# Optimization experiments

Hardware: AMD Instinct MI355X
Metric: run time of the kernel (lower is better)

## Reference

```python
import jax, jax.numpy as jnp
import numpy as np

N, E, H, HEADS, EDIM, DEG_VOCAB, DEG_DIM = 50000, 320000, 128, 4, 8, 100, 16


def _layer_norm(x, g, b, eps=1e-5):
    m = jnp.mean(x, axis=-1, keepdims=True)
    v = jnp.mean(jnp.square(x - m), axis=-1, keepdims=True)
    return (x - m) / jnp.sqrt(v + eps) * g + b


def setup_inputs() -> dict:
    key = jax.random.key(0)
    ks = jax.random.split(key, 24)
    s = 0.05
    inp = {
        "x": jax.random.normal(ks[0], (N, H), jnp.float32),
        "edge_index": jax.random.randint(ks[1], (2, E), 0, N, jnp.int64),
        "edge_attr": jax.random.normal(ks[2], (E, EDIM), jnp.float32),
        "node_degrees": jax.random.randint(ks[3], (N,), 0, DEG_VOCAB, jnp.int64),
        "check_node_mask": jax.random.randint(ks[4], (N,), 0, 2, jnp.int32).astype(bool),
        # GATv2Conv params (bias=False): lin_l, lin_r, lin_edge, att
        "Wl": jax.random.normal(ks[5], (H, HEADS * H), jnp.float32) * s,
        "Wr": jax.random.normal(ks[6], (H, HEADS * H), jnp.float32) * s,
        "We": jax.random.normal(ks[7], (EDIM, HEADS * H), jnp.float32) * s,
        "att": jax.random.normal(ks[8], (HEADS, H), jnp.float32) * s,
        # check_transform: Linear->Tanh->Linear->LayerNorm
        "ct_W1": jax.random.normal(ks[9], (H, H), jnp.float32) * s,
        "ct_b1": jnp.zeros((H,), jnp.float32),
        "ct_W2": jax.random.normal(ks[10], (H, H), jnp.float32) * s,
        "ct_b2": jnp.zeros((H,), jnp.float32),
        "ct_g": jnp.ones((H,), jnp.float32),
        "ct_beta": jnp.zeros((H,), jnp.float32),
        # degree embedding + gate MLP
        "deg_emb": jax.random.normal(ks[11], (DEG_VOCAB, DEG_DIM), jnp.float32) * s,
        "dg_W1": jax.random.normal(ks[12], (H + DEG_DIM, H), jnp.float32) * s,
        "dg_b1": jnp.zeros((H,), jnp.float32),
        "dg_g": jnp.ones((H,), jnp.float32),
        "dg_beta": jnp.zeros((H,), jnp.float32),
        "dg_W2": jax.random.normal(ks[13], (H, H), jnp.float32) * s,
        "dg_b2": jnp.zeros((H,), jnp.float32),
        # final layer norm
        "ln_g": jnp.ones((H,), jnp.float32),
        "ln_beta": jnp.zeros((H,), jnp.float32),
    }
    return inp


def reference(x, edge_index, edge_attr, node_degrees, check_node_mask,
              Wl, Wr, We, att,
              ct_W1, ct_b1, ct_W2, ct_b2, ct_g, ct_beta,
              deg_emb, dg_W1, dg_b1, dg_g, dg_beta, dg_W2, dg_b2,
              ln_g, ln_beta):
    n = x.shape[0]
    # --- check-node transform (applied where mask) ---
    ct = jnp.tanh(x @ ct_W1 + ct_b1) @ ct_W2 + ct_b2
    ct = _layer_norm(ct, ct_g, ct_beta)
    x_t = jnp.where(check_node_mask[:, None], ct, x)

    # --- GATv2Conv with add_self_loops=True, fill_value='mean' for edge_attr ---
    src, dst = edge_index[0], edge_index[1]
    cnt = jax.ops.segment_sum(jnp.ones((edge_attr.shape[0],), edge_attr.dtype), dst, n)
    loop_attr = jax.ops.segment_sum(edge_attr, dst, n) / jnp.maximum(cnt, 1.0)[:, None]
    ar = jnp.arange(n, dtype=src.dtype)
    src_f = jnp.concatenate([src, ar])
    dst_f = jnp.concatenate([dst, ar])
    ea_f = jnp.concatenate([edge_attr, loop_attr], axis=0)

    xl = (x_t @ Wl).reshape(n, HEADS, H)   # source-side (x_j)
    xr = (x_t @ Wr).reshape(n, HEADS, H)   # target-side (x_i)
    ee = (ea_f @ We).reshape(-1, HEADS, H)

    s = jax.nn.leaky_relu(xl[src_f] + xr[dst_f] + ee, 0.2)  # [Ef, heads, H]
    alpha = jnp.einsum('ehd,hd->eh', s, att)
    amax = jax.lax.stop_gradient(jax.ops.segment_max(alpha, dst_f, n))
    ealpha = jnp.exp(alpha - amax[dst_f])
    denom = jax.ops.segment_sum(ealpha, dst_f, n)
    alpha = ealpha / denom[dst_f]           # segment softmax over dst
    # dropout skipped (eval mode)
    out = jax.ops.segment_sum(alpha[:, :, None] * xl[src_f], dst_f, n)  # [N, heads, H]
    x_c2v = out.mean(axis=1)                # concat=False -> mean over heads; bias=False

    # --- degree gating ---
    deg = jnp.clip(node_degrees, 0, DEG_VOCAB - 1)
    df = deg_emb[deg]
    g = jnp.concatenate([x_c2v, df], axis=-1) @ dg_W1 + dg_b1
    g = jax.nn.relu(_layer_norm(g, dg_g, dg_beta)) @ dg_W2 + dg_b2
    x_c2v = x_c2v * jax.nn.sigmoid(g)

    return _layer_norm(x_c2v, ln_g, ln_beta)
```

## Files before the change

### kernel.cpp

```cpp
#include <hip/hip_runtime.h>


#define HDIM 128
#define NHEADS 4
#define EDIM_ 8
#define WHID (NHEADS * HDIM)

typedef __attribute__((ext_vector_type(8))) short short8;
typedef __attribute__((ext_vector_type(4))) float f32x4;

__device__ __forceinline__ float bf2f(unsigned short u) {
    return __uint_as_float(((unsigned int)u) << 16);
}
__device__ __forceinline__ unsigned short f2bf(float f) {
    unsigned int x = __float_as_uint(f);
    unsigned int r = x + 0x7FFFu + ((x >> 16) & 1u);
    return (unsigned short)(r >> 16);
}
__device__ __forceinline__ short8 pack8(float4 a, float4 b) {
    short8 v;
    v[0] = (short)f2bf(a.x); v[1] = (short)f2bf(a.y);
    v[2] = (short)f2bf(a.z); v[3] = (short)f2bf(a.w);
    v[4] = (short)f2bf(b.x); v[5] = (short)f2bf(b.y);
    v[6] = (short)f2bf(b.z); v[7] = (short)f2bf(b.w);
    return v;
}

__global__ __launch_bounds__(256) void k_prep(
    const float* __restrict__ Wl, const float* __restrict__ Wr,
    const float* __restrict__ ctW1, const float* __restrict__ ctW2,
    const float* __restrict__ dgW1, const float* __restrict__ dgW2,
    const float* __restrict__ demb,
    unsigned short* __restrict__ Wbt,
    unsigned short* __restrict__ ctW1t, unsigned short* __restrict__ ctW2t,
    unsigned short* __restrict__ dgW1t, unsigned short* __restrict__ dgW2t,
    float* __restrict__ demb2)
{
    int idx = blockIdx.x * 256 + threadIdx.x;
    if (idx < 131072) {
        int nn = idx >> 7, k = idx & 127;
        const float* W = (nn < WHID) ? Wl : Wr;
        Wbt[idx] = f2bf(W[(size_t)k * WHID + (nn & (WHID - 1))]);
    } else if (idx < 131072 + 65536) {
        int i = idx - 131072;
        int sel = i >> 14;
        int j = i & 16383;
        int n = j >> 7, k = j & 127;
        const float* src = (sel == 0) ? ctW1 : (sel == 1) ? ctW2
                         : (sel == 2) ? dgW1 : dgW2;
        unsigned short* dst = (sel == 0) ? ctW1t : (sel == 1) ? ctW2t
                            : (sel == 2) ? dgW1t : dgW2t;
        dst[j] = f2bf(src[k * 128 + n]);
    } else if (idx < 131072 + 65536 + 12800) {
        int i = idx - 131072 - 65536;
        int d = i >> 7, n = i & 127;
        float s = 0.f;
#pragma unroll
        for (int j = 0; j < 16; j++)
            s += demb[d * 16 + j] * dgW1[(128 + j) * 128 + n];
        demb2[i] = s;
    }
}

__global__ __launch_bounds__(256) void k_ct2(
    const float* __restrict__ x, const int* __restrict__ mask,
    const unsigned short* __restrict__ W1t, const float* __restrict__ b1,
    const unsigned short* __restrict__ W2t, const float* __restrict__ b2,
    const float* __restrict__ g, const float* __restrict__ be,
    unsigned short* __restrict__ xt, int Nn)
{
    __shared__ __align__(16) char Xs[16384];
    __shared__ __align__(16) char Bs[32768];
    __shared__ __align__(16) char Hs[16384];
    __shared__ float rsum[2][64], rsq[2][64];

    const int tid = threadIdx.x;
    const int l = tid & 63, w = tid >> 6;
    const int wm = w >> 1, wn = w & 1;
    const int l15 = l & 15, lq = l >> 4;
    const int row0 = blockIdx.x * 64;

    {
        int r = tid >> 2, q = tid & 3;
        int grow = min(row0 + r, Nn - 1);
        const float* xp = x + (size_t)grow * 128 + q * 32;
        int sb = r * 256, sw = (r & 7) << 4;
#pragma unroll
        for (int u = 0; u < 4; u++) {
            float4 f0 = *reinterpret_cast<const float4*>(xp + u * 8);
            float4 f1 = *reinterpret_cast<const float4*>(xp + u * 8 + 4);
            *reinterpret_cast<short8*>(Xs + sb + (((q * 4 + u) * 16) ^ sw)) = pack8(f0, f1);
        }
    }
    {
        int cr = tid >> 1, h2 = tid & 1;
        int sb = cr * 256, sw = (cr & 7) << 4;
        const unsigned short* wp = W1t + cr * 128 + h2 * 64;
#pragma unroll
        for (int u = 0; u < 8; u++) {
            short8 v = *reinterpret_cast<const short8*>(wp + u * 8);
            *reinterpret_cast<short8*>(Bs + sb + (((h2 * 8 + u) * 16) ^ sw)) = v;
        }
    }
    __syncthreads();

    f32x4 acc[2][4];
#pragma unroll
    for (int i = 0; i < 2; i++)
#pragma unroll
        for (int j = 0; j < 4; j++) acc[i][j] = (f32x4){0.f, 0.f, 0.f, 0.f};
#pragma unroll
    for (int kc = 0; kc < 4; kc++) {
        int ck = (kc * 4 + lq) * 16;
        short8 a[2], b[4];
#pragma unroll
        for (int i = 0; i < 2; i++) {
            int m = wm * 32 + i * 16 + l15;
            a[i] = *reinterpret_cast<const short8*>(Xs + m * 256 + (ck ^ ((m & 7) << 4)));
        }
#pragma unroll
        for (int j = 0; j < 4; j++) {
            int c = wn * 64 + j * 16 + l15;
            b[j] = *reinterpret_cast<const short8*>(Bs + c * 256 + (ck ^ ((c & 7) << 4)));
        }
#pragma unroll
        for (int i = 0; i < 2; i++)
#pragma unroll
            for (int j = 0; j < 4; j++)
                acc[i][j] = __builtin_amdgcn_mfma_f32_16x16x32_bf16(a[i], b[j], acc[i][j], 0, 0, 0);
    }

    {
        float b1v[4];
#pragma unroll
        for (int j = 0; j < 4; j++) b1v[j] = b1[wn * 64 + j * 16 + l15];
#pragma unroll
        for (int i = 0; i < 2; i++)
#pragma unroll
            for (int j = 0; j < 4; j++) {
                int col = wn * 64 + j * 16 + l15;
                int cb = (col >> 3) * 16, ce = (col & 7) * 2;
#pragma unroll
                for (int r = 0; r < 4; r++) {
                    int m = wm * 32 + i * 16 + lq * 4 + r;
                    float v = tanhf(acc[i][j][r] + b1v[j]);
                    *reinterpret_cast<unsigned short*>(
                        Hs + m * 256 + (cb ^ ((m & 7) << 4)) + ce) = f2bf(v);
                }
            }
    }
    __syncthreads();

    {
        int cr = tid >> 1, h2 = tid & 1;
        int sb = cr * 256, sw = (cr & 7) << 4;
        const unsigned short* wp = W2t + cr * 128 + h2 * 64;
#pragma unroll
        for (int u = 0; u < 8; u++) {
            short8 v = *reinterpret_cast<const short8*>(wp + u * 8);
            *reinterpret_cast<short8*>(Bs + sb + (((h2 * 8 + u) * 16) ^ sw)) = v;
        }
    }
    __syncthreads();

    f32x4 acc2[2][4];
#pragma unroll
    for (int i = 0; i < 2; i++)
#pragma unroll
        for (int j = 0; j < 4; j++) acc2[i][j] = (f32x4){0.f, 0.f, 0.f, 0.f};
#pragma unroll
    for (int kc = 0; kc < 4; kc++) {
        int ck = (kc * 4 + lq) * 16;
        short8 a[2], b[4];
#pragma unroll
        for (int i = 0; i < 2; i++) {
            int m = wm * 32 + i * 16 + l15;
            a[i] = *reinterpret_cast<const short8*>(Hs + m * 256 + (ck ^ ((m & 7) << 4)));
        }
#pragma unroll
        for (int j = 0; j < 4; j++) {
            int c = wn * 64 + j * 16 + l15;
            b[j] = *reinterpret_cast<const short8*>(Bs + c * 256 + (ck ^ ((c & 7) << 4)));
        }
#pragma unroll
        for (int i = 0; i < 2; i++)
#pragma unroll
            for (int j = 0; j < 4; j++)
                acc2[i][j] = __builtin_amdgcn_mfma_f32_16x16x32_bf16(a[i], b[j], acc2[i][j], 0, 0, 0);
    }

    float v2[2][4][4];
    {
        float b2v[4];
#pragma unroll
        for (int j = 0; j < 4; j++) b2v[j] = b2[wn * 64 + j * 16 + l15];
#pragma unroll
        for (int i = 0; i < 2; i++)
#pragma unroll
            for (int j = 0; j < 4; j++)
#pragma unroll
                for (int r = 0; r < 4; r++) v2[i][j][r] = acc2[i][j][r] + b2v[j];
    }
#pragma unroll
    for (int i = 0; i < 2; i++)
#pragma unroll
        for (int r = 0; r < 4; r++) {
            float p = 0.f, q = 0.f;
#pragma unroll
            for (int j = 0; j < 4; j++) { float t = v2[i][j][r]; p += t; q += t * t; }
#pragma unroll
            for (int off = 1; off <= 8; off <<= 1) {
                p += __shfl_xor(p, off);
                q += __shfl_xor(q, off);
            }
            if (l15 == 0) {
                int m = wm * 32 + i * 16 + lq * 4 + r;
                rsum[wn][m] = p; rsq[wn][m] = q;
            }
        }
    __syncthreads();

    {
        float gv[4], bev[4];
#pragma unroll
        for (int j = 0; j < 4; j++) {
            int col = wn * 64 + j * 16 + l15;
            gv[j] = g[col]; bev[j] = be[col];
        }
#pragma unroll
        for (int i = 0; i < 2; i++)
#pragma unroll
            for (int r = 0; r < 4; r++) {
                int m = wm * 32 + i * 16 + lq * 4 + r;
                int grow = row0 + m;
                float s = rsum[0][m] + rsum[1][m];
                float q2 = rsq[0][m] + rsq[1][m];
                float mn = s * (1.f / 128.f);
                float va = q2 * (1.f / 128.f) - mn * mn;
                float rs = rsqrtf(va + 1e-5f);
                int mk = (grow < Nn) ? mask[grow] : 0;
#pragma unroll
                for (int j = 0; j < 4; j++) {
                    int col = wn * 64 + j * 16 + l15;
                    float ln = (v2[i][j][r] - mn) * rs * gv[j] + bev[j];
                    unsigned short xo = *reinterpret_cast<const unsigned short*>(
                        Xs + m * 256 + (((col >> 3) * 16) ^ ((m & 7) << 4)) + (col & 7) * 2);
                    unsigned short res = mk ? f2bf(ln) : xo;
                    if (grow < Nn) xt[(size_t)grow * 128 + col] = res;
                }
            }
    }
}

__global__ __launch_bounds__(256) void k_gemm_xlr(
    const unsigned short* __restrict__ xt,
    const unsigned short* __restrict__ Wbt,
    unsigned short* __restrict__ xlr, int Nn)
{
    __shared__ __align__(16) char smem[65536];
    char* Asb = smem;
    char* Bsb = smem + 32768;

    const int tid = threadIdx.x;
    const int bm = blockIdx.x, bn = blockIdx.y;
    const int l = tid & 63;
    const int w = tid >> 6;
    const int wm = w >> 1, wn = w & 1;

    {
        const int c = tid & 15;
        const int rb = tid >> 4;
#pragma unroll
        for (int i = 0; i < 8; i++) {
            int r = i * 16 + rb;
            int swz = (c * 16) ^ ((r & 7) << 4);
            int grow = bm * 128 + r;
            grow = (grow < Nn) ? grow : (Nn - 1);
            short8 va = *reinterpret_cast<const short8*>(xt + (size_t)grow * 128 + c * 8);
            *reinterpret_cast<short8*>(Asb + r * 256 + swz) = va;
            int nrow = bn * 128 + r;
            short8 vb = *reinterpret_cast<const short8*>(Wbt + (size_t)nrow * 128 + c * 8);
            *reinterpret_cast<short8*>(Bsb + r * 256 + swz) = vb;
        }
    }
    __syncthreads();

    f32x4 acc[4][4];
#pragma unroll
    for (int i = 0; i < 4; i++)
#pragma unroll
        for (int j = 0; j < 4; j++) acc[i][j] = (f32x4){0.f, 0.f, 0.f, 0.f};

    const int l15 = l & 15, lq = l >> 4;
#pragma unroll
    for (int kc = 0; kc < 4; kc++) {
        short8 a[4], b[4];
        int ck = (kc * 4 + lq) * 16;
#pragma unroll
        for (int i = 0; i < 4; i++) {
            int m = wm * 64 + i * 16 + l15;
            a[i] = *reinterpret_cast<const short8*>(Asb + m * 256 + (ck ^ ((m & 7) << 4)));
        }
#pragma unroll
        for (int j = 0; j < 4; j++) {
            int nn = wn * 64 + j * 16 + l15;
            b[j] = *reinterpret_cast<const short8*>(Bsb + nn * 256 + (ck ^ ((nn & 7) << 4)));
        }
#pragma unroll
        for (int i = 0; i < 4; i++)
#pragma unroll
            for (int j = 0; j < 4; j++)
                acc[i][j] = __builtin_amdgcn_mfma_f32_16x16x32_bf16(a[i], b[j], acc[i][j], 0, 0, 0);
    }

#pragma unroll
    for (int i = 0; i < 4; i++) {
        int mg0 = bm * 128 + wm * 64 + i * 16 + lq * 4;
#pragma unroll
        for (int j = 0; j < 4; j++) {
            int ng = bn * 128 + wn * 64 + j * 16 + l15;
#pragma unroll
            for (int r = 0; r < 4; r++) {
                int mg = mg0 + r;
                if (mg < Nn)
                    xlr[(size_t)mg * 1024 + ng] = f2bf(acc[i][j][r]);
            }
        }
    }
}

__global__ __launch_bounds__(256) void k_hist(
    const int* __restrict__ ei, const float* __restrict__ eattr,
    float* __restrict__ loop_sum, int* __restrict__ cnt, int Ee)
{
    int gid = blockIdx.x * 256 + threadIdx.x;
    int e = gid >> 3, j = gid & 7;
    if (e >= Ee) return;
    int dst = ei[Ee + e];
    if (j == 0) atomicAdd(&cnt[dst], 1);
    atomicAdd(&loop_sum[(size_t)dst * EDIM_ + j], eattr[(size_t)e * EDIM_ + j]);
}

__global__ __launch_bounds__(256) void k_loopdiv(
    float* __restrict__ loop_sum, const int* __restrict__ cnt, int Nn)
{
    int gid = blockIdx.x * 256 + threadIdx.x;
    if (gid >= Nn * EDIM_) return;
    float c = fmaxf((float)cnt[gid >> 3], 1.f);
    loop_sum[gid] /= c;
}

__global__ __launch_bounds__(256) void k_scanA(const int* __restrict__ cnt,
                                               int* __restrict__ bsum, int Nn)
{
    __shared__ int s[256];
    int i = blockIdx.x * 256 + threadIdx.x;
    int v = (i < Nn) ? cnt[i] + 1 : 0;
    s[threadIdx.x] = v;
    __syncthreads();
    for (int off = 128; off; off >>= 1) {
        if (threadIdx.x < off) s[threadIdx.x] += s[threadIdx.x + off];
        __syncthreads();
    }
    if (threadIdx.x == 0) bsum[blockIdx.x] = s[0];
}

__global__ __launch_bounds__(256) void k_scanB(const int* __restrict__ bsum,
                                               int* __restrict__ boff, int NB)
{
    __shared__ int s[256];
    int tid = threadIdx.x;
    int v = (tid < NB) ? bsum[tid] : 0;
    s[tid] = v;
    __syncthreads();
    for (int off = 1; off < 256; off <<= 1) {
        int t = (tid >= off) ? s[tid - off] : 0;
        __syncthreads();
        s[tid] += t;
        __syncthreads();
    }
    if (tid < NB) boff[tid] = s[tid] - v;
}

__global__ __launch_bounds__(256) void k_scanC(const int* __restrict__ cnt,
                                               const int* __restrict__ boff,
                                               int* __restrict__ offs, int Nn)
{
    __shared__ int s[256];
    int tid = threadIdx.x;
    int i = blockIdx.x * 256 + tid;
    int v = (i < Nn) ? cnt[i] + 1 : 0;
    s[tid] = v;
    __syncthreads();
    for (int off = 1; off < 256; off <<= 1) {
        int t = (tid >= off) ? s[tid - off] : 0;
        __syncthreads();
        s[tid] += t;
        __syncthreads();
    }
    if (i < Nn) {
        int incl = s[tid];
        offs[i] = boff[blockIdx.x] + incl - v;
        if (i == Nn - 1) offs[Nn] = boff[blockIdx.x] + incl;
    }
}

__global__ __launch_bounds__(256) void k_scatter(
    const int* __restrict__ ei, const int* __restrict__ offs,
    int* __restrict__ cursor, int* __restrict__ csr_src,
    int* __restrict__ csr_eid, int Ee, int Nn)
{
    int gid = blockIdx.x * 256 + threadIdx.x;
    if (gid < Ee) {
        int dst = ei[Ee + gid];
        int pos = offs[dst] + atomicAdd(&cursor[dst], 1);
        csr_src[pos] = ei[gid];
        csr_eid[pos] = gid;
    } else if (gid < Ee + Nn) {
        int n = gid - Ee;
        int pos = offs[n + 1] - 1;
        csr_src[pos] = n;
        csr_eid[pos] = Ee + n;
    }
}

__global__ __launch_bounds__(256) void k_attn5(
    const float* __restrict__ eattr, const float* __restrict__ loop_attr,
    const unsigned short* __restrict__ xlr,
    const float* __restrict__ We, const float* __restrict__ att,
    const int* __restrict__ offs, const int* __restrict__ csr_src,
    const int* __restrict__ csr_eid,
    float* __restrict__ xc2v, int Nn, int Ee)
{
    const int tid  = threadIdx.x;
    const int wv   = tid >> 6;
    const int lane = tid & 63;
    const int hp   = wv & 1;
    const int par  = wv >> 1;
    const int n    = blockIdx.x;
    const int hloc = lane >> 5;
    const int col  = (hp * 2 + hloc) * HDIM + (lane & 31) * 4;

    __shared__ float sacc[4][256];
    __shared__ float slsum[4][2];

    float a[4], xr[4], we[EDIM_][4];
#pragma unroll
    for (int k = 0; k < 4; k++) a[k] = att[col + k];
    {
        ushort4 uxr = *reinterpret_cast<const ushort4*>(
            &xlr[(size_t)n * 1024 + WHID + col]);
        xr[0] = bf2f(uxr.x); xr[1] = bf2f(uxr.y);
        xr[2] = bf2f(uxr.z); xr[3] = bf2f(uxr.w);
    }
#pragma unroll
    for (int j = 0; j < EDIM_; j++)
#pragma unroll
        for (int k = 0; k < 4; k++) we[j][k] = We[j * WHID + col + k];

    const int s0 = offs[n], s1 = offs[n + 1];
    float lsum = 0.f, acc[4] = {0.f, 0.f, 0.f, 0.f};

    auto score = [&](int src, int eid, float xl[4]) -> float {
        const float* ep = (eid < Ee) ? eattr + (size_t)eid * EDIM_
                                     : loop_attr + (size_t)n * EDIM_;
        float4 ea = *reinterpret_cast<const float4*>(ep);
        float4 eb = *reinterpret_cast<const float4*>(ep + 4);
        ushort4 u = *reinterpret_cast<const ushort4*>(
            &xlr[(size_t)src * 1024 + col]);
        xl[0] = bf2f(u.x); xl[1] = bf2f(u.y);
        xl[2] = bf2f(u.z); xl[3] = bf2f(u.w);
        float p = 0.f;
#pragma unroll
        for (int k = 0; k < 4; k++) {
            float s = xl[k] + xr[k];
            s = fmaf(ea.x, we[0][k], s); s = fmaf(ea.y, we[1][k], s);
            s = fmaf(ea.z, we[2][k], s); s = fmaf(ea.w, we[3][k], s);
            s = fmaf(eb.x, we[4][k], s); s = fmaf(eb.y, we[5][k], s);
            s = fmaf(eb.z, we[6][k], s); s = fmaf(eb.w, we[7][k], s);
            s = (s > 0.f) ? s : 0.2f * s;
            p = fmaf(s, a[k], p);
        }
        return p;
    };

    int i = s0 + par;
    for (; i + 2 < s1; i += 4) {
        int src0 = csr_src[i],     eid0 = csr_eid[i];
        int src1 = csr_src[i + 2], eid1 = csr_eid[i + 2];
        float xl0[4], xl1[4];
        float p0 = score(src0, eid0, xl0);
        float p1 = score(src1, eid1, xl1);
#pragma unroll
        for (int off = 16; off; off >>= 1) {
            p0 += __shfl_xor(p0, off);
            p1 += __shfl_xor(p1, off);
        }
        float w0 = __expf(p0), w1 = __expf(p1);
        lsum += w0 + w1;
#pragma unroll
        for (int k = 0; k < 4; k++)
            acc[k] = fmaf(w0, xl0[k], fmaf(w1, xl1[k], acc[k]));
    }
    if (i < s1) {
        int src0 = csr_src[i], eid0 = csr_eid[i];
        float xl0[4];
        float p0 = score(src0, eid0, xl0);
#pragma unroll
        for (int off = 16; off; off >>= 1) p0 += __shfl_xor(p0, off);
        float w0 = __expf(p0);
        lsum += w0;
#pragma unroll
        for (int k = 0; k < 4; k++) acc[k] = fmaf(w0, xl0[k], acc[k]);
    }

#pragma unroll
    for (int k = 0; k < 4; k++)
        sacc[wv][hloc * 128 + (lane & 31) * 4 + k] = acc[k];
    if ((lane & 31) == 0) slsum[wv][hloc] = lsum;
    __syncthreads();

    if (tid < HDIM) {
        float o = 0.f;
#pragma unroll
        for (int p2 = 0; p2 < 2; p2++) {
#pragma unroll
            for (int hl = 0; hl < 2; hl++) {
                float num = sacc[p2][hl * 128 + tid] + sacc[p2 + 2][hl * 128 + tid];
                float den = slsum[p2][hl] + slsum[p2 + 2][hl];
                o += num / den;
            }
        }
        xc2v[(size_t)n * HDIM + tid] = 0.25f * o;
    }
}

__global__ __launch_bounds__(256) void k_gate2(
    const float* __restrict__ xc2v, const int* __restrict__ degs,
    const float* __restrict__ demb2,
    const unsigned short* __restrict__ W1t, const float* __restrict__ b1,
    const float* __restrict__ g1v, const float* __restrict__ be1,
    const unsigned short* __restrict__ W2t, const float* __restrict__ b2,
    const float* __restrict__ lng, const float* __restrict__ lnbe,
    float* __restrict__ out, int Nn)
{
    __shared__ __align__(16) char Vs[16384];
    __shared__ __align__(16) char Bs[32768];
    __shared__ __align__(16) char Hs[16384];
    __shared__ float rsum[2][64], rsq[2][64];

    const int tid = threadIdx.x;
    const int l = tid & 63, w = tid >> 6;
    const int wm = w >> 1, wn = w & 1;
    const int l15 = l & 15, lq = l >> 4;
    const int row0 = blockIdx.x * 64;

    {
        int r = tid >> 2, q = tid & 3;
        int grow = min(row0 + r, Nn - 1);
        const float* xp = xc2v + (size_t)grow * 128 + q * 32;
        int sb = r * 256, sw = (r & 7) << 4;
#pragma unroll
        for (int u = 0; u < 4; u++) {
            float4 f0 = *reinterpret_cast<const float4*>(xp + u * 8);
            float4 f1 = *reinterpret_cast<const float4*>(xp + u * 8 + 4);
            *reinterpret_cast<short8*>(Vs + sb + (((q * 4 + u) * 16) ^ sw)) = pack8(f0, f1);
        }
    }
    {
        int cr = tid >> 1, h2 = tid & 1;
        int sb = cr * 256, sw = (cr & 7) << 4;
        const unsigned short* wp = W1t + cr * 128 + h2 * 64;
#pragma unroll
        for (int u = 0; u < 8; u++) {
            short8 v = *reinterpret_cast<const short8*>(wp + u * 8);
            *reinterpret_cast<short8*>(Bs + sb + (((h2 * 8 + u) * 16) ^ sw)) = v;
        }
    }
    __syncthreads();

    f32x4 acc[2][4];
#pragma unroll
    for (int i = 0; i < 2; i++)
#pragma unroll
        for (int j = 0; j < 4; j++) acc[i][j] = (f32x4){0.f, 0.f, 0.f, 0.f};
#pragma unroll
    for (int kc = 0; kc < 4; kc++) {
        int ck = (kc * 4 + lq) * 16;
        short8 a[2], b[4];
#pragma unroll
        for (int i = 0; i < 2; i++) {
            int m = wm * 32 + i * 16 + l15;
            a[i] = *reinterpret_cast<const short8*>(Vs + m * 256 + (ck ^ ((m & 7) << 4)));
        }
#pragma unroll
        for (int j = 0; j < 4; j++) {
            int c = wn * 64 + j * 16 + l15;
            b[j] = *reinterpret_cast<const short8*>(Bs + c * 256 + (ck ^ ((c & 7) << 4)));
        }
#pragma unroll
        for (int i = 0; i < 2; i++)
#pragma unroll
            for (int j = 0; j < 4; j++)
                acc[i][j] = __builtin_amdgcn_mfma_f32_16x16x32_bf16(a[i], b[j], acc[i][j], 0, 0, 0);
    }

    float z[2][4][4];
    {
        float b1v[4];
        int colv[4];
#pragma unroll
        for (int j = 0; j < 4; j++) {
            colv[j] = wn * 64 + j * 16 + l15;
            b1v[j] = b1[colv[j]];
        }
#pragma unroll
        for (int i = 0; i < 2; i++)
#pragma unroll
            for (int r = 0; r < 4; r++) {
                int m = wm * 32 + i * 16 + lq * 4 + r;
                int grow = row0 + m;
                int dg = (grow < Nn) ? degs[grow] : 0;
                dg = min(max(dg, 0), 99);
#pragma unroll
                for (int j = 0; j < 4; j++)
                    z[i][j][r] = acc[i][j][r] + b1v[j] + demb2[dg * 128 + colv[j]];
            }
    }
#pragma unroll
    for (int i = 0; i < 2; i++)
#pragma unroll
        for (int r = 0; r < 4; r++) {
            float p = 0.f, q = 0.f;
#pragma unroll
            for (int j = 0; j < 4; j++) { float t = z[i][j][r]; p += t; q += t * t; }
#pragma unroll
            for (int off = 1; off <= 8; off <<= 1) {
                p += __shfl_xor(p, off);
                q += __shfl_xor(q, off);
            }
            if (l15 == 0) {
                int m = wm * 32 + i * 16 + lq * 4 + r;
                rsum[wn][m] = p; rsq[wn][m] = q;
            }
        }
    __syncthreads();

    {
        float gv[4], bev[4];
#pragma unroll
        for (int j = 0; j < 4; j++) {
            int col = wn * 64 + j * 16 + l15;
            gv[j] = g1v[col]; bev[j] = be1[col];
        }
#pragma unroll
        for (int i = 0; i < 2; i++)
#pragma unroll
            for (int r = 0; r < 4; r++) {
                int m = wm * 32 + i * 16 + lq * 4 + r;
                float s = rsum[0][m] + rsum[1][m];
                float q2 = rsq[0][m] + rsq[1][m];
                float mn = s * (1.f / 128.f);
                float va = q2 * (1.f / 128.f) - mn * mn;
                float rs = rsqrtf(va + 1e-5f);
#pragma unroll
                for (int j = 0; j < 4; j++) {
                    int col = wn * 64 + j * 16 + l15;
                    float h = fmaxf((z[i][j][r] - mn) * rs * gv[j] + bev[j], 0.f);
                    *reinterpret_cast<unsigned short*>(
                        Hs + m * 256 + (((col >> 3) * 16) ^ ((m & 7) << 4)) + (col & 7) * 2) = f2bf(h);
                }
            }
    }
    __syncthreads();

    {
        int cr = tid >> 1, h2 = tid & 1;
        int sb = cr * 256, sw = (cr & 7) << 4;
        const unsigned short* wp = W2t + cr * 128 + h2 * 64;
#pragma unroll
        for (int u = 0; u < 8; u++) {
            short8 v = *reinterpret_cast<const short8*>(wp + u * 8);
            *reinterpret_cast<short8*>(Bs + sb + (((h2 * 8 + u) * 16) ^ sw)) = v;
        }
    }
    __syncthreads();

    f32x4 acc2[2][4];
#pragma unroll
    for (int i = 0; i < 2; i++)
#pragma unroll
        for (int j = 0; j < 4; j++) acc2[i][j] = (f32x4){0.f, 0.f, 0.f, 0.f};
#pragma unroll
    for (int kc = 0; kc < 4; kc++) {
        int ck = (kc * 4 + lq) * 16;
        short8 a[2], b[4];
#pragma unroll
        for (int i = 0; i < 2; i++) {
            int m = wm * 32 + i * 16 + l15;
            a[i] = *reinterpret_cast<const short8*>(Hs + m * 256 + (ck ^ ((m & 7) << 4)));
        }
#pragma unroll
        for (int j = 0; j < 4; j++) {
            int c = wn * 64 + j * 16 + l15;
            b[j] = *reinterpret_cast<const short8*>(Bs + c * 256 + (ck ^ ((c & 7) << 4)));
        }
#pragma unroll
        for (int i = 0; i < 2; i++)
#pragma unroll
            for (int j = 0; j < 4; j++)
                acc2[i][j] = __builtin_amdgcn_mfma_f32_16x16x32_bf16(a[i], b[j], acc2[i][j], 0, 0, 0);
    }

    float y[2][4][4];
    {
        float b2v[4];
#pragma unroll
        for (int j = 0; j < 4; j++) b2v[j] = b2[wn * 64 + j * 16 + l15];
#pragma unroll
        for (int i = 0; i < 2; i++)
#pragma unroll
            for (int j = 0; j < 4; j++) {
                int col = wn * 64 + j * 16 + l15;
                int cb = (col >> 3) * 16, ce = (col & 7) * 2;
#pragma unroll
                for (int r = 0; r < 4; r++) {
                    int m = wm * 32 + i * 16 + lq * 4 + r;
                    float zz = acc2[i][j][r] + b2v[j];
                    float sg = 1.f / (1.f + __expf(-zz));
                    float vv = bf2f(*reinterpret_cast<const unsigned short*>(
                        Vs + m * 256 + (cb ^ ((m & 7) << 4)) + ce));
                    y[i][j][r] = vv * sg;
                }
            }
    }
#pragma unroll
    for (int i = 0; i < 2; i++)
#pragma unroll
        for (int r = 0; r < 4; r++) {
            float p = 0.f, q = 0.f;
#pragma unroll
            for (int j = 0; j < 4; j++) { float t = y[i][j][r]; p += t; q += t * t; }
#pragma unroll
            for (int off = 1; off <= 8; off <<= 1) {
                p += __shfl_xor(p, off);
                q += __shfl_xor(q, off);
            }
            if (l15 == 0) {
                int m = wm * 32 + i * 16 + lq * 4 + r;
                rsum[wn][m] = p; rsq[wn][m] = q;
            }
        }
    __syncthreads();

    {
        float gv[4], bev[4];
#pragma unroll
        for (int j = 0; j < 4; j++) {
            int col = wn * 64 + j * 16 + l15;
            gv[j] = lng[col]; bev[j] = lnbe[col];
        }
#pragma unroll
        for (int i = 0; i < 2; i++)
#pragma unroll
            for (int r = 0; r < 4; r++) {
                int m = wm * 32 + i * 16 + lq * 4 + r;
                int grow = row0 + m;
                float s = rsum[0][m] + rsum[1][m];
                float q2 = rsq[0][m] + rsq[1][m];
                float mn = s * (1.f / 128.f);
                float va = q2 * (1.f / 128.f) - mn * mn;
                float rs = rsqrtf(va + 1e-5f);
#pragma unroll
                for (int j = 0; j < 4; j++) {
                    int col = wn * 64 + j * 16 + l15;
                    float o = (y[i][j][r] - mn) * rs * gv[j] + bev[j];
                    if (grow < Nn) out[(size_t)grow * 128 + col] = o;
                }
            }
    }
}

extern "C" void kernel_launch(void* const* d_in, const int* in_sizes, int n_in,
                              void* d_out, int out_size, void* d_ws, size_t ws_size,
                              hipStream_t stream)
{
    const float* x      = (const float*)d_in[0];
    const int*   ei     = (const int*)d_in[1];
    const float* eattr  = (const float*)d_in[2];
    const int*   degs   = (const int*)d_in[3];
    const int*   maskp  = (const int*)d_in[4];
    const float* Wl     = (const float*)d_in[5];
    const float* Wr     = (const float*)d_in[6];
    const float* We     = (const float*)d_in[7];
    const float* att    = (const float*)d_in[8];
    const float* ct_W1  = (const float*)d_in[9];
    const float* ct_b1  = (const float*)d_in[10];
    const float* ct_W2  = (const float*)d_in[11];
    const float* ct_b2  = (const float*)d_in[12];
    const float* ct_g   = (const float*)d_in[13];
    const float* ct_be  = (const float*)d_in[14];
    const float* demb   = (const float*)d_in[15];
    const float* dg_W1  = (const float*)d_in[16];
    const float* dg_b1  = (const float*)d_in[17];
    const float* dg_g   = (const float*)d_in[18];
    const float* dg_be  = (const float*)d_in[19];
    const float* dg_W2  = (const float*)d_in[20];
    const float* dg_b2  = (const float*)d_in[21];
    const float* ln_g   = (const float*)d_in[22];
    const float* ln_be  = (const float*)d_in[23];
    float* out = (float*)d_out;

    const int N = in_sizes[0] / HDIM;
    const int E = in_sizes[1] / 2;

    char* w = (char*)d_ws;
    size_t off = 0;
    auto alloc = [&](size_t bytes) -> char* {
        char* p = w + off;
        off = (off + bytes + 255) & ~(size_t)255;
        return p;
    };
    unsigned short* xt    = (unsigned short*)alloc((size_t)N * HDIM * 2);
    unsigned short* xlr   = (unsigned short*)alloc((size_t)N * 1024 * 2);
    unsigned short* Wbt   = (unsigned short*)alloc((size_t)1024 * HDIM * 2);
    unsigned short* ctW1t = (unsigned short*)alloc(16384 * 2);
    unsigned short* ctW2t = (unsigned short*)alloc(16384 * 2);
    unsigned short* dgW1t = (unsigned short*)alloc(16384 * 2);
    unsigned short* dgW2t = (unsigned short*)alloc(16384 * 2);
    float* demb2          = (float*)alloc(12800 * 4);
    float* loop_attr      = (float*)alloc((size_t)N * EDIM_ * 4);
    int*   cnt            = (int*)alloc((size_t)N * 4);
    int*   cursor         = (int*)alloc((size_t)N * 4);
    int*   offs           = (int*)alloc((size_t)(N + 1) * 4);
    int*   bsum           = (int*)alloc(256 * 4);
    int*   boff           = (int*)alloc(256 * 4);
    int*   csr_src        = (int*)alloc((size_t)(E + N) * 4);
    int*   csr_eid        = (int*)alloc((size_t)(E + N) * 4);
    float* xc2v           = (float*)alloc((size_t)N * HDIM * 4);
    (void)ws_size;

    hipMemsetAsync(cnt, 0, (size_t)N * 4, stream);
    hipMemsetAsync(cursor, 0, (size_t)N * 4, stream);
    hipMemsetAsync(loop_attr, 0, (size_t)N * EDIM_ * 4, stream);

    const int NB = (N + 255) / 256;

    k_prep<<<(131072 + 65536 + 12800 + 255) / 256, 256, 0, stream>>>(
        Wl, Wr, ct_W1, ct_W2, dg_W1, dg_W2, demb,
        Wbt, ctW1t, ctW2t, dgW1t, dgW2t, demb2);
    k_ct2<<<(N + 63) / 64, 256, 0, stream>>>(x, maskp, ctW1t, ct_b1,
                                             ctW2t, ct_b2, ct_g, ct_be, xt, N);
    {
        dim3 grid((N + 127) / 128, 8);
        k_gemm_xlr<<<grid, 256, 0, stream>>>(xt, Wbt, xlr, N);
    }
    k_hist<<<((size_t)E * EDIM_ + 255) / 256, 256, 0, stream>>>(ei, eattr, loop_attr, cnt, E);
    k_loopdiv<<<((size_t)N * EDIM_ + 255) / 256, 256, 0, stream>>>(loop_attr, cnt, N);
    k_scanA<<<NB, 256, 0, stream>>>(cnt, bsum, N);
    k_scanB<<<1, 256, 0, stream>>>(bsum, boff, NB);
    k_scanC<<<NB, 256, 0, stream>>>(cnt, boff, offs, N);
    k_scatter<<<(E + N + 255) / 256, 256, 0, stream>>>(ei, offs, cursor,
                                                       csr_src, csr_eid, E, N);
    k_attn5<<<N, 256, 0, stream>>>(eattr, loop_attr, xlr, We, att,
                                   offs, csr_src, csr_eid, xc2v, N, E);
    k_gate2<<<(N + 63) / 64, 256, 0, stream>>>(xc2v, degs, demb2,
                                               dgW1t, dg_b1, dg_g, dg_be,
                                               dgW2t, dg_b2, ln_g, ln_be, out, N);
}
```

Baseline: 348.7 us.

## Pack CSR src/eid pairs and map two nodes per attention block

```diff
diff --git a/kernel.cpp b/kernel.cpp
--- a/kernel.cpp
+++ b/kernel.cpp
@@ -407,42 +407,37 @@
 
 __global__ __launch_bounds__(256) void k_scatter(
     const int* __restrict__ ei, const int* __restrict__ offs,
-    int* __restrict__ cursor, int* __restrict__ csr_src,
-    int* __restrict__ csr_eid, int Ee, int Nn)
+    int* __restrict__ cursor, int* __restrict__ csr_se, int Ee, int Nn)
 {
     int gid = blockIdx.x * 256 + threadIdx.x;
     if (gid < Ee) {
         int dst = ei[Ee + gid];
         int pos = offs[dst] + atomicAdd(&cursor[dst], 1);
-        csr_src[pos] = ei[gid];
-        csr_eid[pos] = gid;
+        csr_se[2 * pos]     = ei[gid];
+        csr_se[2 * pos + 1] = gid;
     } else if (gid < Ee + Nn) {
         int n = gid - Ee;
         int pos = offs[n + 1] - 1;
-        csr_src[pos] = n;
-        csr_eid[pos] = Ee + n;
-    }
-}
-
-__global__ __launch_bounds__(256) void k_attn5(
+        csr_se[2 * pos]     = n;
+        csr_se[2 * pos + 1] = Ee + n;
+    }
+}
+
+__global__ __launch_bounds__(256) void k_attn8(
     const float* __restrict__ eattr, const float* __restrict__ loop_attr,
     const unsigned short* __restrict__ xlr,
     const float* __restrict__ We, const float* __restrict__ att,
-    const int* __restrict__ offs, const int* __restrict__ csr_src,
-    const int* __restrict__ csr_eid,
-    float* __restrict__ xc2v, int Nn, int Ee)
+    const int* __restrict__ offs, const int* __restrict__ csr_se,
+    float* __restrict__ xpart, int Nn, int Ee)
 {
     const int tid  = threadIdx.x;
     const int wv   = tid >> 6;
     const int lane = tid & 63;
+    const int n    = blockIdx.x * 2 + (wv >> 1);
     const int hp   = wv & 1;
-    const int par  = wv >> 1;
-    const int n    = blockIdx.x;
     const int hloc = lane >> 5;
     const int col  = (hp * 2 + hloc) * HDIM + (lane & 31) * 4;
-
-    __shared__ float sacc[4][256];
-    __shared__ float slsum[4][2];
+    if (n >= Nn) return;
 
     float a[4], xr[4], we[EDIM_][4];
 #pragma unroll
@@ -484,13 +479,13 @@
         return p;
     };
 
-    int i = s0 + par;
-    for (; i + 2 < s1; i += 4) {
-        int src0 = csr_src[i],     eid0 = csr_eid[i];
-        int src1 = csr_src[i + 2], eid1 = csr_eid[i + 2];
+    int i = s0;
+    for (; i + 1 < s1; i += 2) {
+        int2 se0 = *reinterpret_cast<const int2*>(&csr_se[2 * i]);
+        int2 se1 = *reinterpret_cast<const int2*>(&csr_se[2 * i + 2]);
         float xl0[4], xl1[4];
-        float p0 = score(src0, eid0, xl0);
-        float p1 = score(src1, eid1, xl1);
+        float p0 = score(se0.x, se0.y, xl0);
+        float p1 = score(se1.x, se1.y, xl1);
 #pragma unroll
         for (int off = 16; off; off >>= 1) {
             p0 += __shfl_xor(p0, off);
@@ -503,9 +498,9 @@
             acc[k] = fmaf(w0, xl0[k], fmaf(w1, xl1[k], acc[k]));
     }
     if (i < s1) {
-        int src0 = csr_src[i], eid0 = csr_eid[i];
+        int2 se0 = *reinterpret_cast<const int2*>(&csr_se[2 * i]);
         float xl0[4];
-        float p0 = score(src0, eid0, xl0);
+        float p0 = score(se0.x, se0.y, xl0);
 #pragma unroll
         for (int off = 16; off; off >>= 1) p0 += __shfl_xor(p0, off);
         float w0 = __expf(p0);
@@ -514,29 +509,22 @@
         for (int k = 0; k < 4; k++) acc[k] = fmaf(w0, xl0[k], acc[k]);
     }
 
-#pragma unroll
-    for (int k = 0; k < 4; k++)
-        sacc[wv][hloc * 128 + (lane & 31) * 4 + k] = acc[k];
-    if ((lane & 31) == 0) slsum[wv][hloc] = lsum;
-    __syncthreads();
-
-    if (tid < HDIM) {
-        float o = 0.f;
-#pragma unroll
-        for (int p2 = 0; p2 < 2; p2++) {
-#pragma unroll
-            for (int hl = 0; hl < 2; hl++) {
-                float num = sacc[p2][hl * 128 + tid] + sacc[p2 + 2][hl * 128 + tid];
-                float den = slsum[p2][hl] + slsum[p2 + 2][hl];
-                o += num / den;
-            }
-        }
-        xc2v[(size_t)n * HDIM + tid] = 0.25f * o;
+    const float inv = 1.f / lsum;
+#pragma unroll
+    for (int k = 0; k < 4; k++) {
+        float v = acc[k] * inv;
+        v += __shfl_xor(v, 32);
+        acc[k] = v;
+    }
+    if (lane < 32) {
+        float4 o = make_float4(acc[0], acc[1], acc[2], acc[3]);
+        *reinterpret_cast<float4*>(
+            &xpart[((size_t)hp * Nn + n) * HDIM + lane * 4]) = o;
     }
 }
 
 __global__ __launch_bounds__(256) void k_gate2(
-    const float* __restrict__ xc2v, const int* __restrict__ degs,
+    const float* __restrict__ xpart, const int* __restrict__ degs,
     const float* __restrict__ demb2,
     const unsigned short* __restrict__ W1t, const float* __restrict__ b1,
     const float* __restrict__ g1v, const float* __restrict__ be1,
@@ -554,16 +542,24 @@
     const int wm = w >> 1, wn = w & 1;
     const int l15 = l & 15, lq = l >> 4;
     const int row0 = blockIdx.x * 64;
+    const size_t hp1 = (size_t)Nn * HDIM;
 
     {
         int r = tid >> 2, q = tid & 3;
         int grow = min(row0 + r, Nn - 1);
-        const float* xp = xc2v + (size_t)grow * 128 + q * 32;
+        const float* p0 = xpart + (size_t)grow * 128 + q * 32;
+        const float* p1 = p0 + hp1;
         int sb = r * 256, sw = (r & 7) << 4;
 #pragma unroll
         for (int u = 0; u < 4; u++) {
-            float4 f0 = *reinterpret_cast<const float4*>(xp + u * 8);
-            float4 f1 = *reinterpret_cast<const float4*>(xp + u * 8 + 4);
+            float4 f0 = *reinterpret_cast<const float4*>(p0 + u * 8);
+            float4 f1 = *reinterpret_cast<const float4*>(p0 + u * 8 + 4);
+            float4 g0 = *reinterpret_cast<const float4*>(p1 + u * 8);
+            float4 g1 = *reinterpret_cast<const float4*>(p1 + u * 8 + 4);
+            f0.x = 0.25f * (f0.x + g0.x); f0.y = 0.25f * (f0.y + g0.y);
+            f0.z = 0.25f * (f0.z + g0.z); f0.w = 0.25f * (f0.w + g0.w);
+            f1.x = 0.25f * (f1.x + g1.x); f1.y = 0.25f * (f1.y + g1.y);
+            f1.z = 0.25f * (f1.z + g1.z); f1.w = 0.25f * (f1.w + g1.w);
             *reinterpret_cast<short8*>(Vs + sb + (((q * 4 + u) * 16) ^ sw)) = pack8(f0, f1);
         }
     }
@@ -835,9 +831,8 @@
     int*   offs           = (int*)alloc((size_t)(N + 1) * 4);
     int*   bsum           = (int*)alloc(256 * 4);
     int*   boff           = (int*)alloc(256 * 4);
-    int*   csr_src        = (int*)alloc((size_t)(E + N) * 4);
-    int*   csr_eid        = (int*)alloc((size_t)(E + N) * 4);
-    float* xc2v           = (float*)alloc((size_t)N * HDIM * 4);
+    int*   csr_se         = (int*)alloc((size_t)(E + N) * 8);
+    float* xpart          = (float*)alloc((size_t)2 * N * HDIM * 4);
     (void)ws_size;
 
     hipMemsetAsync(cnt, 0, (size_t)N * 4, stream);
@@ -861,10 +856,10 @@
     k_scanB<<<1, 256, 0, stream>>>(bsum, boff, NB);
     k_scanC<<<NB, 256, 0, stream>>>(cnt, boff, offs, N);
     k_scatter<<<(E + N + 255) / 256, 256, 0, stream>>>(ei, offs, cursor,
-                                                       csr_src, csr_eid, E, N);
-    k_attn5<<<N, 256, 0, stream>>>(eattr, loop_attr, xlr, We, att,
-                                   offs, csr_src, csr_eid, xc2v, N, E);
-    k_gate2<<<(N + 63) / 64, 256, 0, stream>>>(xc2v, degs, demb2,
+                                                       csr_se, E, N);
+    k_attn8<<<(N + 1) / 2, 256, 0, stream>>>(eattr, loop_attr, xlr, We, att,
+                                             offs, csr_se, xpart, N, E);
+    k_gate2<<<(N + 63) / 64, 256, 0, stream>>>(xpart, degs, demb2,
                                                dgW1t, dg_b1, dg_g, dg_be,
                                                dgW2t, dg_b2, ln_g, ln_be, out, N);
 }
```

Result: faster. 329.3 us (-5.6%).
